# Optimization experiments

Hardware: AMD Instinct MI355X
Metric: run time of the kernel (lower is better)

The kernel has to match this reference:

```python
import jax, jax.numpy as jnp
from jax import lax
import numpy as np

SIGMA = 25.0
NUM_STEPS = 100
DT = 0.01
SQRT_DT = float(np.sqrt(DT))


def _score(x, eig, t, cond, W1, we, wt, b1, Wc, W2, b2):
    # x: [B,S,H], eig: [B,S], t: scalar, cond: [B,S,H] or None
    h = x @ W1 + eig[..., None] * we + t * wt + b1
    if cond is not None:
        h = h + cond @ Wc
    h = jax.nn.silu(h)
    return h @ W2 + b2


def _diffuse(x_T, eigvals, eigvecs, cond, params, key):
    # reverse SDE from t=1 to t=0 in NUM_STEPS steps
    ts = jnp.linspace(1.0, 0.0, NUM_STEPS)
    keys = jax.random.split(key, NUM_STEPS)
    VT = jnp.swapaxes(eigvecs, -2, -1)  # [B,S,S]

    def step(x, tk):
        t, k = tk
        x_spec = VT @ x                                   # spectral projection [B,S,H]
        score = _score(x_spec, eigvals, t, cond, *params)
        drift = -(SIGMA ** (2.0 * t)) * score
        noise = jax.random.normal(k, x.shape, x.dtype)
        x_new = x - drift * DT + (SIGMA ** t) * SQRT_DT * noise
        return x_new, None

    x, _ = lax.scan(step, x_T, (ts, keys))
    return x


def _make_net(key, H, scale):
    k = jax.random.split(key, 4)
    return dict(
        W1=jax.random.normal(k[0], (H, H), jnp.float32) * scale,
        we=jax.random.normal(k[1], (H,), jnp.float32) * scale,
        wt=jax.random.normal(k[2], (H,), jnp.float32) * scale,
        b1=jnp.zeros((H,), jnp.float32),
        Wc=jax.random.normal(k[3], (H, H), jnp.float32) * scale,
        W2=jax.random.normal(jax.random.fold_in(key, 99), (H, H), jnp.float32) * scale,
        b2=jnp.zeros((H,), jnp.float32),
    )


def setup_inputs() -> dict:
    key = jax.random.key(0)
    B, S, H = 4, 512, 256
    ks = jax.random.split(key, 9)
    inp = {}
    inp['features_text'] = jax.random.normal(ks[0], (B, S, H), jnp.float32)
    inp['features_audio'] = jax.random.normal(ks[1], (B, S, H), jnp.float32)
    inp['features_visual'] = jax.random.normal(ks[2], (B, S, H), jnp.float32)
    sg = jax.random.normal(ks[3], (B, S, S), jnp.float32)
    inp['speaker_graph'] = 0.5 * (sg + jnp.swapaxes(sg, -2, -1))  # symmetric for eigh
    tg = jax.random.normal(ks[4], (B, S, S), jnp.float32)
    inp['temporal_graph'] = 0.5 * (tg + jnp.swapaxes(tg, -2, -1))
    # only text modality (index 0) is missing -> diffusion path for text only
    inp['missing_mask'] = jnp.zeros((B, S, 3), bool).at[:, :, 0].set(True)
    inp['x_T'] = jax.random.normal(ks[5], (B, S, H), jnp.float32)
    scale = 1.0 / np.sqrt(H)
    for prefix, k in [('ts', ks[6]), ('tt', ks[7])]:  # text_speaker / text_temporal nets
        net = _make_net(k, H, scale)
        for name, v in net.items():
            inp[f'{prefix}_{name}'] = v
    kr = jax.random.split(ks[8], 2)
    inp['rec_W'] = jax.random.normal(kr[0], (H, H), jnp.float32) * scale
    inp['rec_b'] = jnp.zeros((H,), jnp.float32)
    return inp


def reference(features_text, features_audio, features_visual,
              speaker_graph, temporal_graph, missing_mask, x_T,
              ts_W1, ts_we, ts_wt, ts_b1, ts_Wc, ts_W2, ts_b2,
              tt_W1, tt_we, tt_wt, tt_b1, tt_Wc, tt_W2, tt_b2,
              rec_W, rec_b):
    # spectral decomposition of both graphs
    s_vals, s_vecs = jnp.linalg.eigh(speaker_graph)
    t_vals, t_vecs = jnp.linalg.eigh(temporal_graph)

    feats = {'text': features_text, 'audio': features_audio, 'visual': features_visual}
    miss = np.asarray(missing_mask)  # concrete branching as in torch forward
    any_missing = [bool(miss[:, :, i].any()) for i in range(3)]

    params = {'text': (
        (ts_W1, ts_we, ts_wt, ts_b1, ts_Wc, ts_W2, ts_b2),
        (tt_W1, tt_we, tt_wt, tt_b1, tt_Wc, tt_W2, tt_b2))}
    key = jax.random.key(42)

    recovered = {}
    for i, modality in enumerate(['text', 'audio', 'visual']):
        if any_missing[i]:
            # condition = mean of present (non-missing) other modalities
            cond_feats = [feats[m] for j, m in enumerate(['text', 'audio', 'visual'])
                          if m != modality and not any_missing[j]]
            cond = None
            if cond_feats:
                cond = jnp.mean(jnp.stack(cond_feats, axis=-1), axis=-1)
            k_s, k_t = jax.random.split(jax.random.fold_in(key, i))
            p_s, p_t = params[modality]
            x_s = _diffuse(x_T, s_vals, s_vecs, cond, p_s, k_s)
            x_t = _diffuse(x_T, t_vals, t_vecs, cond, p_t, k_t)
            rec = 0.5 * (x_s + x_t)
            recovered[modality] = rec @ rec_W + rec_b
        else:
            recovered[modality] = feats[modality]
    return (recovered['text'], recovered['audio'], recovered['visual'])
```

## Files before the change

### kernel.cpp

```cpp
#include <hip/hip_runtime.h>
#include <math.h>
#include <stdint.h>


#define NT 256
#define SZF 131072
#define MATSZ 262144
#define NB 16
#define ILAST 384
#define TBASE (ILAST+1)
#define TSZ (512-TBASE)

#define BD_DK   0
#define BD_ZK   4096
#define BD_RZK  8192
#define BD_TAU  12288
#define BD_DS   16384
#define BD_RHO  20480
#define BD_KSK  20736
#define BD_KIDX 22784
#define BD_DIDX 24832
#define BD_PERM 26880
#define BD_CNT  28928

#define ALD(p)    __hip_atomic_load((p),  __ATOMIC_RELAXED, __HIP_MEMORY_SCOPE_AGENT)
#define AST(p,v)  __hip_atomic_store((p), (v), __ATOMIC_RELAXED, __HIP_MEMORY_SCOPE_AGENT)

__host__ __device__ static inline unsigned rotl32(unsigned v, int r){ return (v<<r)|(v>>(32-r)); }

__host__ __device__ static inline void tf2x32(unsigned k0, unsigned k1,
                                              unsigned x0, unsigned x1,
                                              unsigned* o0, unsigned* o1){
  unsigned ks2 = k0 ^ k1 ^ 0x1BD11BDAu;
  x0 += k0; x1 += k1;
#define TF4(r0,r1,r2,r3) \
  x0 += x1; x1 = rotl32(x1,r0); x1 ^= x0; \
  x0 += x1; x1 = rotl32(x1,r1); x1 ^= x0; \
  x0 += x1; x1 = rotl32(x1,r2); x1 ^= x0; \
  x0 += x1; x1 = rotl32(x1,r3); x1 ^= x0;
  TF4(13,15,26,6)  x0 += k1;  x1 += ks2 + 1u;
  TF4(17,29,16,24) x0 += ks2; x1 += k0 + 2u;
  TF4(13,15,26,6)  x0 += k0;  x1 += k1 + 3u;
  TF4(17,29,16,24) x0 += k1;  x1 += ks2 + 4u;
  TF4(13,15,26,6)  x0 += ks2; x1 += k0 + 5u;
#undef TF4
  *o0 = x0; *o1 = x1;
}

__device__ static inline float erfinv_xla(float x){
  float w = -log1pf(-x*x);
  float p;
  if (w < 5.0f){
    w -= 2.5f;
    p = 2.81022636e-08f;
    p = fmaf(p, w, 3.43273939e-07f);
    p = fmaf(p, w, -3.5233877e-06f);
    p = fmaf(p, w, -4.39150654e-06f);
    p = fmaf(p, w, 0.00021858087f);
    p = fmaf(p, w, -0.00125372503f);
    p = fmaf(p, w, -0.00417768164f);
    p = fmaf(p, w, 0.246640727f);
    p = fmaf(p, w, 1.50140941f);
  } else {
    w = sqrtf(w) - 3.0f;
    p = -0.000200214257f;
    p = fmaf(p, w, 0.000100950558f);
    p = fmaf(p, w, 0.00134934322f);
    p = fmaf(p, w, -0.00367342844f);
    p = fmaf(p, w, 0.00573950773f);
    p = fmaf(p, w, -0.0076224613f);
    p = fmaf(p, w, 0.00943887047f);
    p = fmaf(p, w, 1.00167406f);
    p = fmaf(p, w, 2.83297682f);
  }
  return p*x;
}

__device__ static inline float bits_to_normal(unsigned bits){
  const float MINV = -0.99999994f;
  float f = __uint_as_float((bits >> 9) | 0x3f800000u) - 1.0f;
  float u = fmaxf(MINV, fmaf(f, 2.0f, MINV));
  return 1.41421356237309515f * erfinv_xla(u);
}

__device__ __forceinline__ void gbar2(unsigned* slots, int sg, int g, unsigned epoch,
                                      int* sdead){
  __threadfence_block();
  __syncthreads();
  int t = threadIdx.x;
  if (t == 0) AST(slots + (sg*NB + g)*16, epoch);
  if (t < NB && !*sdead){
    unsigned* sl = slots + (sg*NB + t)*16;
    int spins = 0;
    while (ALD(sl) < epoch){
      if (++spins > (1<<24)){ *sdead = 1; break; }
      if ((spins & 3) == 0) __builtin_amdgcn_s_sleep(1);
    }
  }
  __syncthreads();
}

__global__ __launch_bounds__(256) void k_sytd2_lds(const float* Gs, const float* Gt,
                                                   double* Vb, double* smalls,
                                                   unsigned* slots, double* Atail){
  int sg = blockIdx.x / NB, g = blockIdx.x % NB;
  const float* G = (sg < 4) ? (Gs + (size_t)sg*MATSZ) : (Gt + (size_t)(sg-4)*MATSZ);
  double* V = Vb + (size_t)sg*MATSZ;
  double* d  = smalls + (size_t)sg*512;
  double* e  = smalls + 4096 + (size_t)sg*512;
  double* tu = smalls + 8192 + (size_t)sg*512;
  double* acc0 = smalls + 274688 + (size_t)sg*512;
  double* acc1 = acc0 + 4096;
  double* col0 = smalls + 282880 + (size_t)sg*512;
  double* col1 = col0 + 4096;
  double* vvh  = smalls + 291072 + (size_t)sg*512;
  double* At = Atail + (size_t)sg*MATSZ;
  int t = threadIdx.x, wave = t >> 6, lane = t & 63;

  __shared__ double Arows[32][512];
  __shared__ double vv[512], wv[512], col2[512], acc[512];
  __shared__ double red[4];
  __shared__ double bc[4];
  __shared__ int sdead;

  if (t == 0) sdead = 0;

  for (int j=0; j<32; j++){
    int r = NB*j + g;
    for (int c=t; c<512; c+=256)
      Arows[j][c] = (double)G[(size_t)r*512 + c];
  }

  for (int r=t; r<512; r+=256) col2[r] = (r>=1) ? (double)G[(size_t)r*512] : 0.0;
  __syncthreads();
  {
    double part = 0.0;
    for (int r=2+t; r<512; r+=256) part += col2[r]*col2[r];
    #pragma unroll
    for (int off=32; off; off>>=1) part += __shfl_down(part, off, 64);
    if (lane==0) red[wave]=part;
    __syncthreads();
    if (t==0){
      double xsq = red[0]+red[1]+red[2]+red[3];
      double alpha = col2[1];
      double beta,tv,scal;
      if (xsq == 0.0){ beta=alpha; tv=0.0; scal=0.0; }
      else {
        beta = -copysign(sqrt(alpha*alpha + xsq), alpha);
        tv = (beta - alpha)/beta;
        scal = 1.0/(alpha - beta);
      }
      if (g==0){ e[0]=beta; tu[0]=tv; }
      bc[0]=tv; bc[1]=scal;
    }
  }
  __syncthreads();
  double tauv = bc[0];
  {
    double scal = bc[1];
    for (int r=t; r<512; r+=256){
      double v = 0.0;
      if (r==1) v = 1.0;
      else if (r>1) v = (tauv==0.0) ? 0.0 : col2[r]*scal;
      vv[r]=v;
      if (r>=1 && (r & (NB-1))==g) V[r] = v;
    }
  }
  __syncthreads();
  if (g==0){
    for (int r=1+t; r<512; r+=256) AST(&col0[r], (double)G[(size_t)r*512 + 1]);
  }
  {
    int r0 = 1 + ((g - 1) & (NB-1));
    for (int r = r0 + NB*wave; r < 512; r += 4*NB){
      const double* Ar = Arows[r>>4];
      double p = 0.0;
      for (int c=lane; c<512; c+=64) p += Ar[c]*vv[c];
      #pragma unroll
      for (int off=32; off; off>>=1) p += __shfl_down(p, off, 64);
      if (lane==0) AST(&acc0[r], p);
    }
  }

  for (int i=0; i<ILAST; i++){
    gbar2(slots, sg, g, (unsigned)(i+1), &sdead);
    int lo=i+1, lo2=i+2;
    double* accR = (i&1) ? acc1 : acc0;
    double* colR = (i&1) ? col1 : col0;
    double* accW = (i&1) ? acc0 : acc1;
    double* colW = (i&1) ? col0 : col1;
    double part = 0.0;
    for (int r=lo+t; r<512; r+=256){
      double a_ = ALD(&accR[r]);
      double c_ = ALD(&colR[r]);
      acc[r]=a_; col2[r]=c_;
      part += (tauv*a_)*vv[r];
    }
    #pragma unroll
    for (int off=32; off; off>>=1) part += __shfl_down(part, off, 64);
    if (lane==0) red[wave]=part;
    __syncthreads();
    {
      double dot = red[0]+red[1]+red[2]+red[3];
      double alpha2 = -0.5*tauv*dot;
      double vlo = vv[lo];
      double wlo = fma(alpha2, vlo, tauv*acc[lo]);
      for (int r=lo+t; r<512; r+=256){
        double wr = fma(alpha2, vv[r], tauv*acc[r]);
        wv[r]=wr;
        col2[r] = col2[r] - vv[r]*wlo - wr*vlo;
      }
    }
    __syncthreads();
    part = 0.0;
    for (int r=lo2+1+t; r<512; r+=256) part += col2[r]*col2[r];
    #pragma unroll
    for (int off=32; off; off>>=1) part += __shfl_down(part, off, 64);
    if (lane==0) red[wave]=part;
    __syncthreads();
    double tau2, scal2;
    {
      double xsq = red[0]+red[1]+red[2]+red[3];
      double alpha = col2[lo2];
      double beta;
      if (xsq == 0.0){ beta=alpha; tau2=0.0; scal2=0.0; }
      else {
        beta = -copysign(sqrt(alpha*alpha + xsq), alpha);
        tau2 = (beta - alpha)/beta;
        scal2 = 1.0/(alpha - beta);
      }
      if (t==0 && g==0){ e[lo]=beta; tu[lo]=tau2; }
    }
    {
      double vvc[8], wvc[8], v2c[8];
      #pragma unroll
      for (int j=0;j<8;j++){
        int c = lo + lane + 64*j;
        bool ok = c < 512;
        vvc[j] = ok ? vv[c] : 0.0;
        wvc[j] = ok ? wv[c] : 0.0;
        double v2v = 0.0;
        if (ok){
          if (c==lo2) v2v = 1.0;
          else if (c>lo2) v2v = (tau2==0.0) ? 0.0 : col2[c]*scal2;
        }
        v2c[j] = v2v;
      }
      int r0 = lo + ((g - lo) & (NB-1));
      for (int r = r0 + NB*wave; r < 512; r += 4*NB){
        double* Ar = Arows[r>>4];
        double vr = vv[r], wr = wv[r];
        double p = 0.0;
        #pragma unroll
        for (int j=0;j<8;j++){
          int c = lo + lane + 64*j;
          if (c < 512){
            double an = Ar[c] - vr*wvc[j] - wr*vvc[j];
            Ar[c] = an;
            p += an * v2c[j];
            if (c == lo2) AST(&colW[r], an);
          }
        }
        #pragma unroll
        for (int off=32; off; off>>=1) p += __shfl_down(p, off, 64);
        if (lane==0) AST(&accW[r], p);
      }
    }
    __syncthreads();
    for (int r=t; r<512; r+=256){
      double v = 0.0;
      if (r==lo2) v = 1.0;
      else if (r>lo2) v = (tau2==0.0) ? 0.0 : col2[r]*scal2;
      vv[r]=v;
      if (r>=lo2 && (r & (NB-1))==g) V[(size_t)lo*512 + r] = v;
    }
    tauv = tau2;
  }

  if (t < 32){
    int r = NB*t + g;
    if (r <= ILAST) d[r] = Arows[t][r];
  }
  for (int j=0; j<32; j++){
    int r = NB*j + g;
    if (r >= TBASE){
      for (int c=TBASE+t; c<512; c+=256)
        At[(size_t)r*512 + c] = Arows[j][c];
    }
  }
  if (g==0){
    for (int r=t; r<512; r+=256) vvh[r] = vv[r];
  }
}

__global__ __launch_bounds__(256) void k_sy_tail(const double* Atail, double* Vb,
                                                 double* smalls){
  int sg = blockIdx.x;
  double* V = Vb + (size_t)sg*MATSZ;
  double* d  = smalls + (size_t)sg*512;
  double* e  = smalls + 4096 + (size_t)sg*512;
  double* tu = smalls + 8192 + (size_t)sg*512;
  const double* accG = smalls + 274688 + (size_t)sg*512;
  const double* colG = smalls + 282880 + (size_t)sg*512;
  const double* vvG  = smalls + 291072 + (size_t)sg*512;
  const double* At0 = Atail + (size_t)sg*MATSZ;
  int t = threadIdx.x, wave = t >> 6, lane = t & 63;

  __shared__ double At[TSZ*128];
  __shared__ double vv[512], wv[512], col2[512], acc[512], accN[512], colN[512];
  __shared__ double red[4];

  for (int rl=0; rl<TSZ; rl++)
    for (int cl=t; cl<TSZ; cl+=256)
      At[rl*128+cl] = At0[(size_t)(TBASE+rl)*512 + TBASE+cl];
  for (int r=t; r<512; r+=256){
    if (r >= ILAST){ vv[r]=vvG[r]; acc[r]=accG[r]; col2[r]=colG[r]; }
  }
  double tauv = tu[ILAST];
  __syncthreads();

  for (int i=ILAST; i<510; i++){
    int lo=i+1, lo2=i+2;
    double part = 0.0;
    for (int r=lo+t; r<512; r+=256) part += (tauv*acc[r])*vv[r];
    #pragma unroll
    for (int off=32; off; off>>=1) part += __shfl_down(part, off, 64);
    if (lane==0) red[wave]=part;
    __syncthreads();
    {
      double dot = red[0]+red[1]+red[2]+red[3];
      double alpha2 = -0.5*tauv*dot;
      double vlo = vv[lo];
      double wlo = fma(alpha2, vlo, tauv*acc[lo]);
      for (int r=lo+t; r<512; r+=256){
        double wr = fma(alpha2, vv[r], tauv*acc[r]);
        wv[r]=wr;
        col2[r] = col2[r] - vv[r]*wlo - wr*vlo;
      }
    }
    __syncthreads();
    part = 0.0;
    for (int r=lo2+1+t; r<512; r+=256) part += col2[r]*col2[r];
    #pragma unroll
    for (int off=32; off; off>>=1) part += __shfl_down(part, off, 64);
    if (lane==0) red[wave]=part;
    __syncthreads();
    double tau2, scal2;
    {
      double xsq = red[0]+red[1]+red[2]+red[3];
      double alpha = col2[lo2];
      double beta;
      if (xsq == 0.0){ beta=alpha; tau2=0.0; scal2=0.0; }
      else {
        beta = -copysign(sqrt(alpha*alpha + xsq), alpha);
        tau2 = (beta - alpha)/beta;
        scal2 = 1.0/(alpha - beta);
      }
      if (t==0){ e[lo]=beta; tu[lo]=tau2; }
    }
    {
      double vvc[8], wvc[8], v2c[8];
      #pragma unroll
      for (int j=0;j<8;j++){
        int c = lo + lane + 64*j;
        bool ok = c < 512;
        vvc[j] = ok ? vv[c] : 0.0;
        wvc[j] = ok ? wv[c] : 0.0;
        double v2v = 0.0;
        if (ok){
          if (c==lo2) v2v = 1.0;
          else if (c>lo2) v2v = (tau2==0.0) ? 0.0 : col2[c]*scal2;
        }
        v2c[j] = v2v;
      }
      for (int r = lo + wave; r < 512; r += 4){
        double* Ar = &At[(r-TBASE)*128];
        double vr = vv[r], wr = wv[r];
        double p = 0.0;
        #pragma unroll
        for (int j=0;j<8;j++){
          int c = lo + lane + 64*j;
          if (c < 512){
            double an = Ar[c-TBASE] - vr*wvc[j] - wr*vvc[j];
            Ar[c-TBASE] = an;
            p += an * v2c[j];
            if (c == lo2) colN[r] = an;
          }
        }
        #pragma unroll
        for (int off=32; off; off>>=1) p += __shfl_down(p, off, 64);
        if (lane==0) accN[r] = p;
      }
    }
    __syncthreads();
    for (int r=t; r<512; r+=256){
      if (r >= lo2){
        double v = (r==lo2) ? 1.0 : ((tau2==0.0) ? 0.0 : col2[r]*scal2);
        vv[r]=v;
        V[(size_t)lo*512 + r] = v;
        col2[r] = colN[r];
        acc[r] = accN[r];
      }
    }
    tauv = tau2;
    __syncthreads();
  }
  for (int rl=t; rl<TSZ; rl+=256) d[TBASE+rl] = At[rl*128+rl];
}

__global__ void k_scale(double* smalls, int sbase){
  int sg = sbase + blockIdx.x, t = threadIdx.x;
  double* d = smalls + (size_t)sg*512;
  double* e = smalls + 4096 + (size_t)sg*512;
  __shared__ double red[256];
  double m = 0.0;
  for (int i=t;i<512;i+=256) m = fmax(m, fabs(d[i]));
  for (int i=t;i<511;i+=256) m = fmax(m, fabs(e[i]));
  red[t]=m; __syncthreads();
  for (int off=128; off; off>>=1){ if (t<off) red[t]=fmax(red[t],red[t+off]); __syncthreads(); }
  double org = red[0]; if (org == 0.0) org = 1.0;
  if (t==0) smalls[12288+sg] = org;
  double inv = 1.0/org;
  __syncthreads();
  for (int i=t;i<512;i+=256) d[i] *= inv;
  for (int i=t;i<511;i+=256) e[i] *= inv;
  __syncthreads();
  if (t < 31){
    int k = t + 1;
    double ae = fabs(e[16*k - 1]);
    d[16*k - 1] -= ae;
    d[16*k]     -= ae;
  }
}

__global__ __launch_bounds__(256) void k_leaves(double* smalls, double* Zb, int sbase){
  __shared__ double LA[4][256];
  __shared__ double LQ[4][256];
  int t = threadIdx.x, w = t >> 6, lane = t & 63;
  int L = blockIdx.x*4 + w;
  int s_local = L >> 5;
  int sg = sbase + s_local;
  int leaf = L & 31;
  double* dd = smalls + (size_t)sg*512;
  double* ee = smalls + 4096 + (size_t)sg*512;
  double* Z = Zb + (size_t)s_local*MATSZ;
  int base = leaf*16;
  double* A = LA[w]; double* Q = LQ[w];

  for (int i=lane; i<256; i+=64){ A[i]=0.0; Q[i]=0.0; }
  __builtin_amdgcn_sched_barrier(0);
  if (lane < 16){ A[lane*17] = dd[base+lane]; Q[lane*17] = 1.0; }
  if (lane < 15){
    double ev = ee[base+lane];
    A[lane*16+lane+1] = ev; A[(lane+1)*16+lane] = ev;
  }
  __builtin_amdgcn_sched_barrier(0);
  double nr = 0.0;
  if (lane == 0){ for (int i=0;i<256;i++) nr += A[i]*A[i]; }
  nr = __shfl(nr, 0, 64);
  double thr = nr*1e-30 + 1e-300;

  for (int sweep=0; sweep<60; sweep++){
    double offs = 0.0;
    for (int p=0;p<15;p++) for (int q=p+1;q<16;q++){
      double apq = A[p*16+q];
      offs += 2.0*apq*apq;
      if (apq == 0.0) continue;
      double theta = 0.5*(A[q*17]-A[p*17])/apq;
      double tt;
      if (fabs(theta) > 1e18) tt = 0.5/theta;
      else tt = copysign(1.0, theta)/(fabs(theta)+sqrt(theta*theta+1.0));
      double cc = 1.0/sqrt(tt*tt+1.0), ss = tt*cc;
      __builtin_amdgcn_sched_barrier(0);
      if (lane < 16){
        int k = lane;
        double akp=A[k*16+p], akq=A[k*16+q];
        A[k*16+p] = cc*akp - ss*akq;
        A[k*16+q] = ss*akp + cc*akq;
      }
      __builtin_amdgcn_sched_barrier(0);
      if (lane < 16){
        int k = lane;
        double apk=A[p*16+k], aqk=A[q*16+k];
        A[p*16+k] = cc*apk - ss*aqk;
        A[q*16+k] = ss*apk + cc*aqk;
      }
      __builtin_amdgcn_sched_barrier(0);
      if (lane < 16){
        int k = lane;
        double qkp=Q[k*16+p], qkq=Q[k*16+q];
        Q[k*16+p] = cc*qkp - ss*qkq;
        Q[k*16+q] = ss*qkp + cc*qkq;
      }
      __builtin_amdgcn_sched_barrier(0);
    }
    if (offs < thr) break;
  }
  __builtin_amdgcn_sched_barrier(0);
  if (lane == 0){
    for (int i=0;i<16;i++){
      int mi=i;
      for (int j=i+1;j<16;j++) if (A[j*17] < A[mi*17]) mi=j;
      if (mi!=i){
        double tmp=A[i*17]; A[i*17]=A[mi*17]; A[mi*17]=tmp;
        for (int k=0;k<16;k++){ double q1=Q[k*16+i]; Q[k*16+i]=Q[k*16+mi]; Q[k*16+mi]=q1; }
      }
    }
  }
  __builtin_amdgcn_sched_barrier(0);
  if (lane < 16) dd[base+lane] = A[lane*17];
  for (int i=lane; i<256; i+=64){
    int r = i >> 4, c = i & 15;
    Z[(size_t)(base+r)*512 + base + c] = Q[i];
  }
}

__global__ __launch_bounds__(256) void k_deflate(double* smalls, const double* Zsrc_b,
                                                 double* bscr, int level, int sbase){
  const double EPS32 = 5.9604644775390625e-8;
  const double ISQ2  = 0.70710678118654752440;
  int s_local = blockIdx.x;
  int sg = sbase + s_local;
  int hh = 16 << level, n = hh << 1;
  int merge = blockIdx.y, start = merge*n;
  double* d = smalls + (size_t)sg*512;
  const double* e = smalls + 4096 + (size_t)sg*512;
  const double* Z = Zsrc_b + (size_t)s_local*MATSZ;
  double* rotg = smalls + 12544 + (size_t)(sg*32+merge)*1024;
  double* dkG  = bscr + BD_DK  + (size_t)s_local*512 + start;
  double* zkG  = bscr + BD_ZK  + (size_t)s_local*512 + start;
  double* rzkG = bscr + BD_RZK + (size_t)s_local*512 + start;
  double* dsG  = bscr + BD_DS  + (size_t)s_local*512 + start;
  double* rhoG = bscr + BD_RHO;
  int* kidxG = (int*)(bscr + BD_KIDX) + s_local*512 + start;
  int* didxG = (int*)(bscr + BD_DIDX) + s_local*512 + start;
  int* permG = (int*)(bscr + BD_PERM) + s_local*512 + start;
  int* cntG  = (int*)(bscr + BD_CNT) + (s_local*32+merge)*2;

  __shared__ double ds[512], zl[512];
  __shared__ double rc[256], rs[256];
  __shared__ double red[256];
  __shared__ double sv[2];
  __shared__ int perm[512], kidx[512], didx[512];
  __shared__ int rp[256], rq[256];
  __shared__ int counts[2];
  int t = threadIdx.x;
  if (t == 0){
    int i=0, j=hh, k=0;
    while (i < hh && j < n){
      if (d[start+i] <= d[start+j]) perm[k++]=i++; else perm[k++]=j++;
    }
    while (i < hh) perm[k++]=i++;
    while (j < n)  perm[k++]=j++;
  }
  __syncthreads();
  double eb = e[start+hh-1];
  double rho = 2.0*fabs(eb);
  double sgn = (eb < 0.0) ? -1.0 : 1.0;
  for (int i=t; i<n; i+=NT){
    int p = perm[i];
    ds[i] = d[start+p];
    double zr = (p < hh) ? Z[(size_t)(start+hh-1)*512 + start + p]
                         : sgn * Z[(size_t)(start+hh)*512 + start + p];
    zl[i] = zr * ISQ2;
  }
  __syncthreads();
  double m = 0.0;
  for (int i=t;i<n;i+=NT) m = fmax(m, fabs(zl[i]));
  red[t]=m; __syncthreads();
  for (int off=128; off; off>>=1){ if (t<off) red[t]=fmax(red[t],red[t+off]); __syncthreads(); }
  if (t==0) sv[0] = red[0];
  __syncthreads();
  m = 0.0;
  for (int i=t;i<n;i+=NT) m = fmax(m, fabs(ds[i]));
  red[t]=m; __syncthreads();
  for (int off=128; off; off>>=1){ if (t<off) red[t]=fmax(red[t],red[t+off]); __syncthreads(); }
  if (t==0) sv[1] = red[0];
  __syncthreads();
  double zmaxv = sv[0];
  double tol = 8.0*EPS32*fmax(sv[1], zmaxv);

  if (t == 0){
    int K=0, nd=0, nrot=0;
    if (rho*zmaxv <= tol){
      for (int j=0;j<n;j++) didx[nd++]=j;
    } else {
      int pj = -1;
      for (int j=0;j<n;j++){
        if (rho*fabs(zl[j]) <= tol){
          didx[nd++]=j;
        } else if (pj < 0){
          pj = j;
        } else {
          double s_ = zl[pj], c_ = zl[j];
          double tau2 = sqrt(c_*c_ + s_*s_);
          double tdf = ds[j] - ds[pj];
          double cc = c_/tau2, sr = -s_/tau2;
          if (fabs(tdf*cc*sr) <= tol){
            zl[j] = tau2; zl[pj] = 0.0;
            if (nrot < 256){
              rp[nrot]=perm[pj]; rq[nrot]=perm[j]; rc[nrot]=cc; rs[nrot]=sr; nrot++;
            }
            double tn = ds[pj]*cc*cc + ds[j]*sr*sr;
            ds[j]  = ds[pj]*sr*sr + ds[j]*cc*cc;
            ds[pj] = tn;
            didx[nd++] = pj;
            pj = j;
          } else {
            kidx[K++] = pj;
            pj = j;
          }
        }
      }
      if (pj >= 0) kidx[K++] = pj;
    }
    for (int a=1;a<nd;a++){
      int v = didx[a]; double dv = ds[v]; int b = a-1;
      while (b >= 0 && ds[didx[b]] > dv){ didx[b+1]=didx[b]; b--; }
      didx[b+1] = v;
    }
    counts[0]=K; counts[1]=nd;
    cntG[0]=K; cntG[1]=nd;
    rhoG[s_local*32+merge] = rho;
    rotg[0] = (double)nrot;
    for (int i=0;i<nrot;i++){
      rotg[1+4*i]=(double)rp[i]; rotg[2+4*i]=(double)rq[i];
      rotg[3+4*i]=rc[i]; rotg[4+4*i]=rs[i];
    }
  }
  __syncthreads();
  int K = counts[0], nd = counts[1];
  for (int k=t; k<K; k+=NT){
    int ki = kidx[k];
    double dv = ds[ki], zv = zl[ki];
    dkG[k]=dv; zkG[k]=zv; rzkG[k]=(rho*zv)*zv; kidxG[k]=ki;
  }
  for (int j=t; j<n;  j+=NT){ dsG[j]=ds[j]; permG[j]=perm[j]; }
  for (int j=t; j<nd; j+=NT) didxG[j]=didx[j];
}

__global__ __launch_bounds__(256) void k_bisect(double* bscr, int level, int split){
  int s_local = blockIdx.x;
  int hh = 16 << level, n = hh << 1;
  int merge = blockIdx.y, start = merge*n;
  const double* dkG  = bscr + BD_DK  + (size_t)s_local*512 + start;
  const double* zkG  = bscr + BD_ZK  + (size_t)s_local*512 + start;
  const double* rzkG = bscr + BD_RZK + (size_t)s_local*512 + start;
  double* taukG = bscr + BD_TAU + (size_t)s_local*512 + start;
  int* KskG = (int*)(bscr + BD_KSK) + s_local*512 + start;
  const int* cntG = (int*)(bscr + BD_CNT) + (s_local*32+merge)*2;
  double rho = (bscr + BD_RHO)[s_local*32+merge];
  __shared__ double dks[512], rzks[512], zks[512];
  int t = threadIdx.x;
  int K = cntG[0];
  for (int i=t;i<K;i+=NT){ dks[i]=dkG[i]; rzks[i]=rzkG[i]; zks[i]=zkG[i]; }
  __syncthreads();
  int lane = t & 63, w = t >> 6;
  for (int j2 = blockIdx.z*4 + w; j2 < K; j2 += split*4){
    int Kb; double lo, hi;
    if (j2 < K-1){
      double mid = 0.5*(dks[j2+1]-dks[j2]);
      double dj = dks[j2];
      double part = 0.0;
      for (int i=lane;i<K;i+=64){ double dif=(dks[i]-dj)-mid; part += rzks[i]/dif; }
      #pragma unroll
      for (int off=32; off; off>>=1) part += __shfl_xor(part, off, 64);
      double gg = 1.0 + part;
      if (gg >= 0.0){ Kb=j2;   lo=0.0;  hi=mid; }
      else          { Kb=j2+1; lo=-mid; hi=0.0; }
    } else {
      double part = 0.0;
      for (int i=lane;i<K;i+=64) part += zks[i]*zks[i];
      #pragma unroll
      for (int off=32; off; off>>=1) part += __shfl_xor(part, off, 64);
      Kb=K-1; lo=0.0; hi=rho*part + 1e-300;
    }
    double dK = dks[Kb];
    for (int it=0; it<72; it++){
      double mid = 0.5*(lo+hi);
      if (mid==lo || mid==hi) break;
      double part = 0.0;
      for (int i=lane;i<K;i+=64){ double dif=(dks[i]-dK)-mid; part += rzks[i]/dif; }
      #pragma unroll
      for (int off=32; off; off>>=1) part += __shfl_xor(part, off, 64);
      double gg = 1.0 + part;
      if (gg < 0.0) lo=mid; else hi=mid;
    }
    if (lane==0){ KskG[j2]=Kb; taukG[j2]=0.5*(lo+hi); }
  }
}

__global__ __launch_bounds__(256) void k_sfin(double* smalls, double* Sm_b,
                                              const double* bscr, int level, int sbase){
  int s_local = blockIdx.x;
  int sg = sbase + s_local;
  int hh = 16 << level, n = hh << 1;
  int merge = blockIdx.y, start = merge*n;
  double* d = smalls + (size_t)sg*512;
  double* Sm = Sm_b + (size_t)s_local*MATSZ;
  const double* rotg = smalls + 12544 + (size_t)(sg*32+merge)*1024;
  const double* dkG  = bscr + BD_DK  + (size_t)s_local*512 + start;
  const double* zkG  = bscr + BD_ZK  + (size_t)s_local*512 + start;
  const double* taukG= bscr + BD_TAU + (size_t)s_local*512 + start;
  const double* dsG  = bscr + BD_DS  + (size_t)s_local*512 + start;
  const int* KskG = (int*)(bscr + BD_KSK) + s_local*512 + start;
  const int* kidxG= (int*)(bscr + BD_KIDX) + s_local*512 + start;
  const int* didxG= (int*)(bscr + BD_DIDX) + s_local*512 + start;
  const int* permG= (int*)(bscr + BD_PERM) + s_local*512 + start;
  const int* cntG = (int*)(bscr + BD_CNT) + (s_local*32+merge)*2;
  double rho = (bscr + BD_RHO)[s_local*32+merge];
  __shared__ double dk[512], zk[512], tauk[512], zh[512], outlam[512], ds[512];
  __shared__ int Ksk[512], kidx[512], didx[512], perm[512], outid[512];
  int t = threadIdx.x;
  int K = cntG[0], nd = cntG[1];
  for (int i=t;i<K;i+=NT){
    dk[i]=dkG[i]; zk[i]=zkG[i]; tauk[i]=taukG[i]; Ksk[i]=KskG[i]; kidx[i]=kidxG[i];
  }
  for (int i=t;i<n;i+=NT){ ds[i]=dsG[i]; perm[i]=permG[i]; }
  for (int i=t;i<nd;i+=NT) didx[i]=didxG[i];
  __syncthreads();
  for (int i=t; i<K; i+=NT){
    double P = (Ksk[i]==i) ? tauk[i] : (dk[Ksk[i]]-dk[i]) + tauk[i];
    for (int j=0;j<K;j++){
      if (j==i) continue;
      double num = (dk[Ksk[j]]-dk[i]) + tauk[j];
      double den = dk[j]-dk[i];
      P *= num/den;
    }
    zh[i] = copysign(sqrt(fabs(P/rho)), zk[i]);
  }
  __syncthreads();
  if (t == 0){
    int a=0, b=0;
    for (int j=0;j<n;j++){
      double la = (a<K)  ? (dk[Ksk[a]]+tauk[a]) : 1e300;
      double lb = (b<nd) ? ds[didx[b]]          : 1e300;
      if (la <= lb){ outid[j]=a;     outlam[j]=la; a++; }
      else         { outid[j]=512+b; outlam[j]=lb; b++; }
    }
  }
  __syncthreads();
  for (int j=t; j<n; j+=NT) d[start+j] = outlam[j];
  for (int j=t; j<n; j+=NT){
    double* col = Sm + (size_t)(start+j)*512;
    int id = outid[j];
    for (int i=0;i<n;i++) col[i]=0.0;
    if (id >= 512){
      col[perm[didx[id-512]]] = 1.0;
    } else {
      int k = id;
      double ss_ = 0.0;
      for (int i=0;i<K;i++){
        double dif = (dk[i]-dk[Ksk[k]]) - tauk[k];
        if (dif == 0.0) dif = 1e-300;
        double v = zh[i]/dif;
        col[perm[kidx[i]]] = v; ss_ += v*v;
      }
      double inv = 1.0/sqrt(ss_);
      for (int i=0;i<K;i++) col[perm[kidx[i]]] *= inv;
    }
  }
  int cnt = (int)rotg[0];
  if (cnt > 0){
    for (int j=t; j<n; j+=NT){
      double* col = Sm + (size_t)(start+j)*512;
      for (int i=cnt-1; i>=0; i--){
        int p = (int)rotg[1+4*i], q = (int)rotg[2+4*i];
        double c = rotg[3+4*i], sr = rotg[4+4*i];
        double a = col[p], b = col[q];
        col[p] = c*a - sr*b;
        col[q] = sr*a + c*b;
      }
    }
  }
}

__global__ __launch_bounds__(256) void k_gemm64(const double* Zsrc_b, const double* Sm_b,
                                                double* Zdst_b, int level){
  int hh = 16 << level, n = hh << 1;
  int mpm = 512 / n;
  int bz = blockIdx.z;
  int s = bz / mpm, merge = bz % mpm;
  int start = merge*n;
  const double* Zs = Zsrc_b + (size_t)s*MATSZ;
  const double* Sm = Sm_b + (size_t)s*MATSZ;
  double* Zd = Zdst_b + (size_t)s*MATSZ;
  int row0 = start + blockIdx.y*32, col0 = start + blockIdx.x*32;
  int t = threadIdx.x;
  int tr = t >> 4, tc = t & 15;
  __shared__ double As[32][33];
  __shared__ double Bs[32][33];
  double a00=0,a01=0,a10=0,a11=0;
  for (int q0=0; q0<n; q0+=32){
    #pragma unroll
    for (int it=0; it<4; it++){
      int idx = t + it*256;
      int r = idx >> 5, q = idx & 31;
      As[r][q] = Zs[(size_t)(row0+r)*512 + start + q0 + q];
    }
    #pragma unroll
    for (int it=0; it<4; it++){
      int idx = t + it*256;
      int c = idx >> 5, q = idx & 31;
      Bs[q][c] = Sm[(size_t)(col0+c)*512 + q0 + q];
    }
    __syncthreads();
    #pragma unroll 8
    for (int q=0;q<32;q++){
      double ar0=As[tr][q], ar1=As[tr+16][q];
      double bc0=Bs[q][tc], bc1=Bs[q][tc+16];
      a00 = fma(ar0,bc0,a00); a01 = fma(ar0,bc1,a01);
      a10 = fma(ar1,bc0,a10); a11 = fma(ar1,bc1,a11);
    }
    __syncthreads();
  }
  Zd[(size_t)(row0+tr)*512 + col0+tc]       = a00;
  Zd[(size_t)(row0+tr)*512 + col0+tc+16]    = a01;
  Zd[(size_t)(row0+tr+16)*512 + col0+tc]    = a10;
  Zd[(size_t)(row0+tr+16)*512 + col0+tc+16] = a11;
}

__global__ __launch_bounds__(256) void k_backq(double* Z2_b, const double* Vh_b,
                                               const double* smalls, int sbase){
  int s_local = blockIdx.x, cb = blockIdx.y;
  int sg = sbase + s_local;
  double* Z = Z2_b + (size_t)s_local*MATSZ;
  const double* V = Vh_b + (size_t)sg*MATSZ;
  const double* tu = smalls + 8192 + (size_t)sg*512;
  int cg = threadIdx.x >> 5, lane = threadIdx.x & 31;
  int c = cb*8 + cg;
  __shared__ double zc[8][512];
  for (int r=lane; r<512; r+=32) zc[cg][r] = Z[(size_t)r*512 + c];
  for (int i=509; i>=0; i--){
    double tv = tu[i];
    if (tv == 0.0) continue;
    double wp = 0.0;
    for (int r=i+1+lane; r<512; r+=32) wp += V[(size_t)i*512 + r]*zc[cg][r];
    #pragma unroll
    for (int off=16; off; off>>=1) wp += __shfl_down(wp, off, 32);
    double w = __shfl(wp, 0, 32);
    double tw = tv*w;
    for (int r=i+1+lane; r<512; r+=32) zc[cg][r] -= tw*V[(size_t)i*512 + r];
  }
  for (int r=lane; r<512; r+=32) Z[(size_t)r*512 + c] = zc[cg][r];
}

__global__ void k_finalize(const double* Z2_b, const double* smalls,
                           float* Vs32, float* Vt32, float* eig, int sbase){
  int s_local = blockIdx.x;
  int sg = sbase + s_local;
  const double* Z = Z2_b + (size_t)s_local*MATSZ;
  float* Vt_pass = (sg < 4) ? (Vs32 + (size_t)sg*MATSZ)
                            : (Vt32 + (size_t)(sg-4)*MATSZ);
  double org = smalls[12288+sg];
  int idx = blockIdx.y*256 + threadIdx.x;
  int r = idx >> 9, c = idx & 511;
  Vt_pass[(size_t)c*512 + r] = (float)Z[(size_t)r*512 + c];
  if (idx < 512)
    eig[(size_t)sg*512 + idx] = (float)(smalls[(size_t)sg*512 + idx]*org);
}

struct KArgs {
  const float* Vt;
  const float* Vt2;
  float *xspec, *hbuf, *x, *E;
  const float *W1s, *W1t, *W2s, *W2t;
  const float *b2s, *b2t, *wts, *wtt, *b1s, *b1t, *wes, *wet;
  const float *cond, *Wcs, *Wct;
  const float *eig;
  const float *rec, *recW, *recb;
  float* out;
  float t, a, bc;
  unsigned nk0, nk1, nk2, nk3;
  int mode, nmat, ntx;
};

__global__ __launch_bounds__(256) void k_gemm32(KArgs P){
  int t = threadIdx.x;
  int L = blockIdx.x;
  int mat = L % P.nmat;
  int tile = L / P.nmat;
  int n0 = (tile % P.ntx) << 5;
  int m0 = (tile / P.ntx) << 6;
  const float *A, *B; float *C;
  int lda, K, chain = 0;
  if (P.mode == 0){
    A = (mat < 4) ? (P.Vt + (size_t)mat*MATSZ) : (P.Vt2 + (size_t)(mat-4)*MATSZ);
    lda = 512; K = 512;
    B = P.x + (size_t)mat*SZF; C = P.xspec + (size_t)mat*SZF;
  } else if (P.mode == 1){
    chain = mat >> 2;
    A = P.xspec + (size_t)mat*SZF; lda = 256; K = 256;
    B = chain ? P.W1t : P.W1s; C = P.hbuf + (size_t)mat*SZF;
  } else if (P.mode == 2){
    chain = mat >> 2;
    A = P.hbuf + (size_t)mat*SZF; lda = 256; K = 256;
    B = chain ? P.W2t : P.W2s; C = P.x + (size_t)mat*SZF;
  } else if (P.mode == 3){
    chain = mat;
    A = P.cond; lda = 256; K = 256;
    B = chain ? P.Wct : P.Wcs; C = P.E + (size_t)chain*4*SZF;
  } else {
    A = P.rec; lda = 256; K = 256;
    B = P.recW; C = P.out;
  }
  __shared__ float As[2][32][68];
  __shared__ float Bs[2][32][36];
  float acc[4][2] = {{0}};
  const int ra = t >> 2, kk4 = (t & 3) << 2;
  const int kb = (t & 127) >> 3, c4 = (t & 7) << 2;
  const int tr4 = (t >> 4) << 2, tc2 = (t & 15) << 1;
  const float* Aptr = &A[(size_t)(m0 + ra)*lda + kk4];
  const float* Bptr = &B[(size_t)kb*256 + n0 + c4];
  {
    const float4 av  = *(const float4*)Aptr;
    const float4 av2 = *(const float4*)(Aptr + 16);
    As[0][kk4+0][ra]=av.x;  As[0][kk4+1][ra]=av.y;  As[0][kk4+2][ra]=av.z;  As[0][kk4+3][ra]=av.w;
    As[0][16+kk4+0][ra]=av2.x; As[0][16+kk4+1][ra]=av2.y; As[0][16+kk4+2][ra]=av2.z; As[0][16+kk4+3][ra]=av2.w;
    if (t < 128){
      const float4 bv  = *(const float4*)Bptr;
      const float4 bv2 = *(const float4*)(Bptr + (size_t)16*256);
      *(float4*)&Bs[0][kb][c4] = bv;
      *(float4*)&Bs[0][kb+16][c4] = bv2;
    }
  }
  int buf = 0;
  for (int k0=0; k0<K; k0+=32){
    __syncthreads();
    bool more = (k0+32) < K;
    float4 avN, avN2, bvN, bvN2;
    if (more){
      avN  = *(const float4*)(Aptr + k0 + 32);
      avN2 = *(const float4*)(Aptr + k0 + 48);
      if (t < 128){
        bvN  = *(const float4*)(Bptr + (size_t)(k0+32)*256);
        bvN2 = *(const float4*)(Bptr + (size_t)(k0+48)*256);
      }
    }
    {
      const float (*Asb)[68] = As[buf];
      const float (*Bsb)[36] = Bs[buf];
      #pragma unroll
      for (int kk=0; kk<32; kk++){
        const float4 a4 = *(const float4*)&Asb[kk][tr4];
        const float2 b2 = *(const float2*)&Bsb[kk][tc2];
        const float ar[4] = {a4.x, a4.y, a4.z, a4.w};
        #pragma unroll
        for (int q=0;q<4;q++){
          acc[q][0] = fmaf(ar[q], b2.x, acc[q][0]);
          acc[q][1] = fmaf(ar[q], b2.y, acc[q][1]);
        }
      }
    }
    if (more){
      int nb = buf^1;
      As[nb][kk4+0][ra]=avN.x;  As[nb][kk4+1][ra]=avN.y;  As[nb][kk4+2][ra]=avN.z;  As[nb][kk4+3][ra]=avN.w;
      As[nb][16+kk4+0][ra]=avN2.x; As[nb][16+kk4+1][ra]=avN2.y; As[nb][16+kk4+2][ra]=avN2.z; As[nb][16+kk4+3][ra]=avN2.w;
      if (t < 128){
        *(float4*)&Bs[nb][kb][c4] = bvN;
        *(float4*)&Bs[nb][kb+16][c4] = bvN2;
      }
      buf = nb;
    }
  }
  #pragma unroll
  for (int q=0;q<4;q++){
    int r = m0 + tr4 + q;
    size_t rowoff = (size_t)r*256 + n0 + tc2;
    float2 cv;
    if (P.mode == 2) cv = *(const float2*)&C[rowoff];
    float res[2];
    #pragma unroll
    for (int p=0;p<2;p++){
      int c = n0 + tc2 + p;
      size_t oi = (size_t)r*256 + c;
      float v = acc[q][p];
      if (P.mode == 1){
        v += P.E[(size_t)mat*SZF + oi] + P.t * ((chain ? P.wtt : P.wts)[c]);
        float sg = 1.0f/(1.0f + expf(-v));
        v = v * sg;
      } else if (P.mode == 2){
        float bias = (chain ? P.b2t : P.b2s)[c];
        unsigned j = ((unsigned)(mat & 3))*131072u + (unsigned)oi;
        unsigned kk0 = chain ? P.nk2 : P.nk0;
        unsigned kk1 = chain ? P.nk3 : P.nk1;
        unsigned y0, y1;
        tf2x32(kk0, kk1, 0u, j, &y0, &y1);
        float nz = bits_to_normal(y0 ^ y1);
        float cx = (p==0) ? cv.x : cv.y;
        v = cx + P.a*(v + bias) + P.bc*nz;
      } else if (P.mode == 3){
        int bb = r >> 9, s2 = r & 511;
        v += (chain ? P.b1t : P.b1s)[c]
           + P.eig[(size_t)(chain*4 + bb)*512 + s2] * ((chain ? P.wet : P.wes)[c]);
      } else if (P.mode == 4){
        v += P.recb[c];
      }
      res[p] = v;
    }
    *(float2*)&C[rowoff] = make_float2(res[0], res[1]);
  }
}

__global__ void k_init(float* cond, float* x, const float* a, const float* v,
                       const float* xT){
  size_t i = (size_t)blockIdx.x*256 + threadIdx.x;
  size_t b = i >> 17, off = i & 131071;
  x[i] = xT[((b & 3) << 17) + off];
  if (i < 524288) cond[i] = 0.5f*(a[i] + v[i]);
}

__global__ void k_recc(float* rec, const float* x, float* out,
                       const float* a, const float* v){
  size_t i = (size_t)blockIdx.x*256 + threadIdx.x;
  if (i < 524288) rec[i] = 0.5f*(x[i] + x[i + 524288]);
  out[524288 + i] = (i < 524288) ? a[i] : v[i - 524288];
}

extern "C" void kernel_launch(void* const* d_in, const int* in_sizes, int n_in,
                              void* d_out, int out_size, void* d_ws, size_t ws_size,
                              hipStream_t stream){
  const float* f_audio   = (const float*)d_in[1];
  const float* f_visual  = (const float*)d_in[2];
  const float* g_speaker = (const float*)d_in[3];
  const float* g_temporal= (const float*)d_in[4];
  const float* x_T       = (const float*)d_in[6];
  const float* tsW1=(const float*)d_in[7],  *tswe=(const float*)d_in[8],
             * tswt=(const float*)d_in[9],  *tsb1=(const float*)d_in[10],
             * tsWc=(const float*)d_in[11], *tsW2=(const float*)d_in[12],
             * tsb2=(const float*)d_in[13];
  const float* ttW1=(const float*)d_in[14], *ttwe=(const float*)d_in[15],
             * ttwt=(const float*)d_in[16], *ttb1=(const float*)d_in[17],
             * ttWc=(const float*)d_in[18], *ttW2=(const float*)d_in[19],
             * ttb2=(const float*)d_in[20];
  const float* recW=(const float*)d_in[21], *recb=(const float*)d_in[22];
  float* out = (float*)d_out;

  const size_t MB = 1ull << 20;
  if (ws_size < 43*MB) return;
  bool wide = ws_size >= 80*MB;

  char* ws = (char*)d_ws;
  double* Vh     = (double*)(ws + 0);
  double* Atail  = (double*)(ws + 16*MB);
  double* A64    = (double*)(ws + 16*MB);
  double* Zb     = wide ? (double*)(ws + 48*MB) : (double*)(ws + 24*MB);
  double* Sm     = wide ? (double*)(ws + 64*MB) : (double*)(ws + 32*MB);
  double* smalls = (double*)(ws + 40*MB);
  unsigned* slots = (unsigned*)(smalls + 295168);
  float* Vt32_s  = (float*)(ws + 0);
  float* Vt32_t  = (float*)(ws + 8*MB);
  float* eig32   = (float*)(ws + 42*MB + 512*1024);
  double* bscr   = (double*)(ws + 42*MB + 640*1024);
  float* cond  = (float*)(ws + 16*MB);
  float* E     = (float*)(ws + 18*MB);
  float* xall  = (float*)(ws + 22*MB);
  float* xspec = (float*)(ws + 26*MB);
  float* hbuf  = (float*)(ws + 30*MB);

  unsigned f0, f1;
  tf2x32(0u, 42u, 0u, 0u, &f0, &f1);
  unsigned s0,s1,t0,t1;
  tf2x32(f0, f1, 0u, 0u, &s0, &s1);
  tf2x32(f0, f1, 0u, 1u, &t0, &t1);
  unsigned skeys[100][2], tkeys[100][2];
  for (int k=0; k<100; k++){
    tf2x32(s0, s1, 0u, (unsigned)k, &skeys[k][0], &skeys[k][1]);
    tf2x32(t0, t1, 0u, (unsigned)k, &tkeys[k][0], &tkeys[k][1]);
  }

  hipMemsetAsync(slots, 0, 16384, stream);

  k_sytd2_lds<<<8*NB, 256, 0, stream>>>(g_speaker, g_temporal, Vh, smalls, slots, Atail);
  k_sy_tail<<<8, 256, 0, stream>>>(Atail, Vh, smalls);

  int npass = wide ? 1 : 2;
  int nmat  = wide ? 8 : 4;
  for (int pass=0; pass<npass; pass++){
    int sbase = wide ? 0 : 4*pass;
    k_scale<<<nmat, 256, 0, stream>>>(smalls, sbase);
    hipMemsetAsync(Zb, 0, (size_t)(wide?16:8)*MB, stream);
    hipMemsetAsync(A64, 0, (size_t)(wide?16:8)*MB, stream);
    k_leaves<<<nmat*8, 256, 0, stream>>>(smalls, Zb, sbase);
    for (int level=0; level<5; level++){
      int n = 32 << level, mpm = 512/n;
      double* src = (level & 1) ? A64 : Zb;
      double* dst = (level & 1) ? Zb  : A64;
      int split = 2 << level;
      k_deflate<<<dim3(nmat, mpm), 256, 0, stream>>>(smalls, src, bscr, level, sbase);
      k_bisect<<<dim3(nmat, mpm, split), 256, 0, stream>>>(bscr, level, split);
      k_sfin<<<dim3(nmat, mpm), 256, 0, stream>>>(smalls, Sm, bscr, level, sbase);
      k_gemm64<<<dim3(n/32, n/32, nmat*mpm), 256, 0, stream>>>(src, Sm, dst, level);
    }
    k_backq<<<dim3(nmat, 64), 256, 0, stream>>>(A64, Vh, smalls, sbase);
    k_finalize<<<dim3(nmat, 1024), 256, 0, stream>>>(A64, smalls,
                                                     Vt32_s, Vt32_t, eig32, sbase);
  }

  k_init<<<4096, 256, 0, stream>>>(cond, xall, f_audio, f_visual, x_T);

  KArgs P;
  P.Vt = Vt32_s; P.Vt2 = Vt32_t;
  P.xspec = xspec; P.hbuf = hbuf; P.x = xall; P.E = E;
  P.W1s = tsW1; P.W1t = ttW1; P.W2s = tsW2; P.W2t = ttW2;
  P.b2s = tsb2; P.b2t = ttb2; P.wts = tswt; P.wtt = ttwt;
  P.b1s = tsb1; P.b1t = ttb1; P.wes = tswe; P.wet = ttwe;
  P.cond = cond; P.Wcs = tsWc; P.Wct = ttWc;
  P.eig = eig32; P.rec = xspec; P.recW = recW; P.recb = recb; P.out = out;
  P.t = 0.f; P.a = 0.f; P.bc = 0.f;
  P.nk0 = 0; P.nk1 = 0; P.nk2 = 0; P.nk3 = 0;
  P.ntx = 8;

  P.mode = 3; P.nmat = 2;
  k_gemm32<<<512, 256, 0, stream>>>(P);

  for (int k=0; k<100; k++){
    float tf = (float)(1.0 - (double)k/99.0);
    float av = (float)(pow(25.0, 2.0*(double)tf) * 0.01);
    float bcv = (float)(pow(25.0, (double)tf) * 0.1);
    P.nk0 = skeys[k][0]; P.nk1 = skeys[k][1];
    P.nk2 = tkeys[k][0]; P.nk3 = tkeys[k][1];
    P.nmat = 8;
    P.mode = 0;
    k_gemm32<<<512, 256, 0, stream>>>(P);
    P.mode = 1; P.t = tf;
    k_gemm32<<<512, 256, 0, stream>>>(P);
    P.mode = 2; P.a = av; P.bc = bcv;
    k_gemm32<<<512, 256, 0, stream>>>(P);
  }

  k_recc<<<4096, 256, 0, stream>>>(xspec, xall, out, f_audio, f_visual);
  P.mode = 4; P.nmat = 1;
  k_gemm32<<<256, 256, 0, stream>>>(P);
}
```

Before: 14.17 ms.

## Split grid barrier into early signal and late wait; tile finalize transpose

The per-iteration cross-block barrier in the tridiagonalization loop is split so each block publishes its epoch right after the trailing update, before building the next Householder vector, and waits only at the top of the next iteration. This lets the vector construction overlap with other blocks' arrival. The Givens rotation pass in the secular-equation finalize is merged into the per-column loop, removing a second sweep over the columns. The finalize kernel now transposes through a 32x32 shared-memory tile, so reads and writes are both coalesced and four times fewer blocks are launched. The early signal relies on no later work in the iteration touching data that other blocks read.

Result: no change. 14.07 ms, median of 2 (-0.7%).

```diff
diff --git a/kernel.cpp b/kernel.cpp
--- a/kernel.cpp
+++ b/kernel.cpp
@@ -83,23 +83,6 @@
   return 1.41421356237309515f * erfinv_xla(u);
 }
 
-__device__ __forceinline__ void gbar2(unsigned* slots, int sg, int g, unsigned epoch,
-                                      int* sdead){
-  __threadfence_block();
-  __syncthreads();
-  int t = threadIdx.x;
-  if (t == 0) AST(slots + (sg*NB + g)*16, epoch);
-  if (t < NB && !*sdead){
-    unsigned* sl = slots + (sg*NB + t)*16;
-    int spins = 0;
-    while (ALD(sl) < epoch){
-      if (++spins > (1<<24)){ *sdead = 1; break; }
-      if ((spins & 3) == 0) __builtin_amdgcn_s_sleep(1);
-    }
-  }
-  __syncthreads();
-}
-
 __global__ __launch_bounds__(256) void k_sytd2_lds(const float* Gs, const float* Gt,
                                                    double* Vb, double* smalls,
                                                    unsigned* slots, double* Atail){
@@ -181,9 +164,19 @@
       if (lane==0) AST(&acc0[r], p);
     }
   }
+  __syncthreads();
+  if (t == 0) AST(slots + (sg*NB + g)*16, 1u);
 
   for (int i=0; i<ILAST; i++){
-    gbar2(slots, sg, g, (unsigned)(i+1), &sdead);
+    if (t < NB && !sdead){
+      unsigned* sl = slots + (sg*NB + t)*16;
+      int spins = 0;
+      while (ALD(sl) < (unsigned)(i+1)){
+        if (++spins > (1<<24)){ sdead = 1; break; }
+        if ((spins & 3) == 0) __builtin_amdgcn_s_sleep(1);
+      }
+    }
+    __syncthreads();
     int lo=i+1, lo2=i+2;
     double* accR = (i&1) ? acc1 : acc0;
     double* colR = (i&1) ? col1 : col0;
@@ -267,6 +260,7 @@
       }
     }
     __syncthreads();
+    if (t == 0) AST(slots + (sg*NB + g)*16, (unsigned)(i+2));
     for (int r=t; r<512; r+=256){
       double v = 0.0;
       if (r==lo2) v = 1.0;
@@ -741,6 +735,7 @@
   }
   __syncthreads();
   for (int j=t; j<n; j+=NT) d[start+j] = outlam[j];
+  int cnt = (int)rotg[0];
   for (int j=t; j<n; j+=NT){
     double* col = Sm + (size_t)(start+j)*512;
     int id = outid[j];
@@ -759,18 +754,12 @@
       double inv = 1.0/sqrt(ss_);
       for (int i=0;i<K;i++) col[perm[kidx[i]]] *= inv;
     }
-  }
-  int cnt = (int)rotg[0];
-  if (cnt > 0){
-    for (int j=t; j<n; j+=NT){
-      double* col = Sm + (size_t)(start+j)*512;
-      for (int i=cnt-1; i>=0; i--){
-        int p = (int)rotg[1+4*i], q = (int)rotg[2+4*i];
-        double c = rotg[3+4*i], sr = rotg[4+4*i];
-        double a = col[p], b = col[q];
-        col[p] = c*a - sr*b;
-        col[q] = sr*a + c*b;
-      }
+    for (int i=cnt-1; i>=0; i--){
+      int p = (int)rotg[1+4*i], q = (int)rotg[2+4*i];
+      double c = rotg[3+4*i], sr = rotg[4+4*i];
+      double a = col[p], b = col[q];
+      col[p] = c*a - sr*b;
+      col[q] = sr*a + c*b;
     }
   }
 }
@@ -852,12 +841,31 @@
   const double* Z = Z2_b + (size_t)s_local*MATSZ;
   float* Vt_pass = (sg < 4) ? (Vs32 + (size_t)sg*MATSZ)
                             : (Vt32 + (size_t)(sg-4)*MATSZ);
-  double org = smalls[12288+sg];
-  int idx = blockIdx.y*256 + threadIdx.x;
-  int r = idx >> 9, c = idx & 511;
-  Vt_pass[(size_t)c*512 + r] = (float)Z[(size_t)r*512 + c];
-  if (idx < 512)
-    eig[(size_t)sg*512 + idx] = (float)(smalls[(size_t)sg*512 + idx]*org);
+  int t = threadIdx.x;
+  int tr = blockIdx.y & 15, tc = blockIdx.y >> 4;
+  __shared__ float ft[32][33];
+  {
+    int i = t >> 3, j4 = (t & 7) << 2;
+    const double* zr = &Z[(size_t)(tr*32 + i)*512 + tc*32 + j4];
+    ft[i][j4+0] = (float)zr[0];
+    ft[i][j4+1] = (float)zr[1];
+    ft[i][j4+2] = (float)zr[2];
+    ft[i][j4+3] = (float)zr[3];
+  }
+  __syncthreads();
+  {
+    int j = t >> 3, i4 = (t & 7) << 2;
+    float* vr = &Vt_pass[(size_t)(tc*32 + j)*512 + tr*32 + i4];
+    vr[0] = ft[i4+0][j];
+    vr[1] = ft[i4+1][j];
+    vr[2] = ft[i4+2][j];
+    vr[3] = ft[i4+3][j];
+  }
+  if (blockIdx.y == 0){
+    double org = smalls[12288+sg];
+    for (int idx=t; idx<512; idx+=256)
+      eig[(size_t)sg*512 + idx] = (float)(smalls[(size_t)sg*512 + idx]*org);
+  }
 }
 
 struct KArgs {
@@ -1093,8 +1101,8 @@
       k_gemm64<<<dim3(n/32, n/32, nmat*mpm), 256, 0, stream>>>(src, Sm, dst, level);
     }
     k_backq<<<dim3(nmat, 64), 256, 0, stream>>>(A64, Vh, smalls, sbase);
-    k_finalize<<<dim3(nmat, 1024), 256, 0, stream>>>(A64, smalls,
-                                                     Vt32_s, Vt32_t, eig32, sbase);
+    k_finalize<<<dim3(nmat, 256), 256, 0, stream>>>(A64, smalls,
+                                                    Vt32_s, Vt32_t, eig32, sbase);
   }
 
   k_init<<<4096, 256, 0, stream>>>(cond, xall, f_audio, f_visual, x_T);
```
